# Optimization experiments

Measured on AMD Instinct MI355X. Metric: run time of the kernel, lower is better.

## Reference

```python
import jax, jax.numpy as jnp
import numpy as np

N_NODES = 100000
N_EDGES = 3200000
NUM_GRAPHS = 64
NEG_SLOPE = 0.2  # PyG GATConv default leaky_relu slope


def gat_conv(x, src, dst, W, att_src, att_dst, bias, heads, out_ch, concat):
    """PyG GATConv (default args: add_self_loops=True, negative_slope=0.2).
    src/dst already include self loops."""
    n = x.shape[0]
    h = (x @ W).reshape(n, heads, out_ch)              # [N,H,C]
    a_src = jnp.sum(h * att_src, axis=-1)              # [N,H]
    a_dst = jnp.sum(h * att_dst, axis=-1)              # [N,H]
    e = jax.nn.leaky_relu(a_src[src] + a_dst[dst], NEG_SLOPE)  # [E,H]
    # segment softmax over destination nodes
    m = jax.ops.segment_max(e, dst, num_segments=n)
    ex = jnp.exp(e - m[dst])
    denom = jax.ops.segment_sum(ex, dst, num_segments=n)
    alpha = ex / (denom[dst] + 1e-16)                  # [E,H]
    msg = h[src] * alpha[:, :, None]                   # [E,H,C]
    out = jax.ops.segment_sum(msg, dst, num_segments=n)  # [N,H,C]
    if concat:
        out = out.reshape(n, heads * out_ch)
    else:
        out = out.mean(axis=1)
    return out + bias


def setup_inputs() -> dict:
    key = jax.random.key(0)
    ks = jax.random.split(key, 12)
    x = jax.random.normal(ks[0], (N_NODES, 4), dtype=jnp.float32)
    edge_index = jax.random.randint(ks[1], (2, N_EDGES), 0, N_NODES, dtype=jnp.int64)
    batch = jnp.sort(jax.random.randint(ks[2], (N_NODES,), 0, NUM_GRAPHS, dtype=jnp.int64))
    s = 0.1
    return {
        "x": x,
        "edge_index": edge_index,
        "batch": batch,
        "W1": jax.random.normal(ks[3], (4, 64), dtype=jnp.float32) * s,
        "att_src1": jax.random.normal(ks[4], (2, 32), dtype=jnp.float32) * s,
        "att_dst1": jax.random.normal(ks[5], (2, 32), dtype=jnp.float32) * s,
        "bias1": jnp.zeros((64,), dtype=jnp.float32),
        "W2": jax.random.normal(ks[6], (64, 64), dtype=jnp.float32) * s,
        "att_src2": jax.random.normal(ks[7], (1, 64), dtype=jnp.float32) * s,
        "att_dst2": jax.random.normal(ks[8], (1, 64), dtype=jnp.float32) * s,
        "bias2": jnp.zeros((64,), dtype=jnp.float32),
    }


def reference(x, edge_index, batch, W1, att_src1, att_dst1, bias1, W2, att_src2, att_dst2, bias2):
    n = x.shape[0]
    loops = jnp.arange(n, dtype=edge_index.dtype)
    src = jnp.concatenate([edge_index[0], loops])
    dst = jnp.concatenate([edge_index[1], loops])
    h = gat_conv(x, src, dst, W1, att_src1, att_dst1, bias1, heads=2, out_ch=32, concat=True)
    h = jax.nn.elu(h)
    # dropout is identity in eval mode
    h = gat_conv(h, src, dst, W2, att_src2, att_dst2, bias2, heads=1, out_ch=64, concat=False)
    # global_mean_pool
    sums = jax.ops.segment_sum(h, batch, num_segments=NUM_GRAPHS)
    counts = jax.ops.segment_sum(jnp.ones((n,), h.dtype), batch, num_segments=NUM_GRAPHS)
    return sums / jnp.maximum(counts, 1.0)[:, None]
```

## Files before the change

kernel.cpp:

```cpp
#include <hip/hip_runtime.h>
#include <hip/hip_bf16.h>
#include <hip/hip_fp16.h>
#include <math.h>


__device__ __forceinline__ float leaky(float x) { return x >= 0.f ? x : 0.2f * x; }
__device__ __forceinline__ int iclamp(int v, int lo, int hi) {
  return v < lo ? lo : (v > hi ? hi : v);
}
__device__ __forceinline__ unsigned char f8(float v) {
  return (unsigned char)(__builtin_amdgcn_cvt_pk_fp8_f32(v, v, 0, false) & 0xff);
}
__device__ __forceinline__ float hlo(unsigned w) {
  __half2 h = *(__half2*)&w; return __half2float(h.x);
}
__device__ __forceinline__ float hhi(unsigned w) {
  __half2 h = *(__half2*)&w; return __half2float(h.y);
}

typedef __attribute__((ext_vector_type(8))) _Float16 f16x8;
typedef __attribute__((ext_vector_type(4))) float f32x4;
typedef __attribute__((ext_vector_type(2))) float f32x2;

#define NBUCK 1024
#define BSHIFT 7
#define BCAP 4608
#define CSRSZ (NBUCK * BCAP)
#define MAXR 8
#define SCAP (MAXR * 1024)

__global__ __launch_bounds__(1024, 8) void k_scatt(
    const int* __restrict__ ei, int E, int n, int* __restrict__ bcur,
    unsigned* __restrict__ pairs,
    const float* __restrict__ x, const float* __restrict__ W1,
    const float* __restrict__ att_src1, const float* __restrict__ att_dst1,
    uint4* __restrict__ xs, float* __restrict__ a_dst1, int NBK) {
  __shared__ int h[NBUCK];
  __shared__ int cur[NBUCK];
  __shared__ int gofs[NBUCK];
  __shared__ int wtot[16];
  __shared__ int htot;
  __shared__ unsigned sstage[SCAP];
  __shared__ unsigned short sbkt[SCAP];
  __shared__ float W1s[256];
  __shared__ float as1[64];
  __shared__ float ad1[64];
  int t = threadIdx.x;
  if (blockIdx.x >= NBK) {
    if (t < 256) W1s[t] = W1[t];
    else if (t >= 256 && t < 320) as1[t - 256] = att_src1[t - 256];
    else if (t >= 320 && t < 384) ad1[t - 320] = att_dst1[t - 320];
    __syncthreads();
    int grp = t >> 4, sub = t & 15;
    int node = (blockIdx.x - NBK) * 64 + grp;
    if (node >= n) return;
    float4 xr = ((const float4*)x)[node];
    float vs = 0.f, vd = 0.f;
    #pragma unroll
    for (int i = 0; i < 4; ++i) {
      int c = sub * 4 + i;
      float hv = xr.x * W1s[c] + xr.y * W1s[64 + c] + xr.z * W1s[128 + c] + xr.w * W1s[192 + c];
      vs = fmaf(hv, as1[c], vs);
      vd = fmaf(hv, ad1[c], vd);
    }
    #pragma unroll
    for (int m = 4; m >= 1; m >>= 1) { vs += __shfl_xor(vs, m); vd += __shfl_xor(vd, m); }
    int wl = t & 63;
    float vs1 = __shfl(vs, (wl & 48) + 8);
    float vd1 = __shfl(vd, (wl & 48) + 8);
    if (sub == 0) {
      __half2 x01 = __float22half2_rn(make_float2(xr.x, xr.y));
      __half2 x23 = __float22half2_rn(make_float2(xr.z, xr.w));
      uint4 rec;
      rec.x = *(unsigned*)&x01;
      rec.y = *(unsigned*)&x23;
      rec.z = __float_as_uint(vs);
      rec.w = __float_as_uint(vs1);
      xs[node] = rec;
      ((float2*)a_dst1)[node] = make_float2(vd, vd1);
    }
    return;
  }
  h[t] = 0;
  __syncthreads();
  int chunk = (E + NBK - 1) / NBK;
  int beg = blockIdx.x * chunk;
  int end = beg + chunk; if (end > E) end = E;
  unsigned pR[MAXR];
  unsigned short bR[MAXR];
  int cntr = 0;
  for (int i = beg + t; i < end && cntr < MAXR; i += 1024) {
    int s = iclamp(ei[i], 0, n - 1);
    int d = iclamp(ei[E + i], 0, n - 1);
    int bkt = d >> BSHIFT;
    pR[cntr] = ((unsigned)(d & 127) << 25) | (unsigned)s;
    bR[cntr] = (unsigned short)bkt;
    atomicAdd(&h[bkt], 1);
    ++cntr;
  }
  __syncthreads();
  int v = h[t];
  int lanei = t & 63, wid = t >> 6;
  int sc = v;
  #pragma unroll
  for (int ofs = 1; ofs < 64; ofs <<= 1) {
    int u = __shfl_up(sc, ofs);
    if (lanei >= ofs) sc += u;
  }
  if (lanei == 63) wtot[wid] = sc;
  __syncthreads();
  if (wid == 0 && lanei < 16) {
    int wv = wtot[lanei];
    int s2 = wv;
    #pragma unroll
    for (int ofs = 1; ofs < 16; ofs <<= 1) {
      int u = __shfl_up(s2, ofs);
      if (lanei >= ofs) s2 += u;
    }
    wtot[lanei] = s2 - wv;
  }
  __syncthreads();
  int incl = sc + wtot[wid];
  int loff = incl - v;
  cur[t] = loff;
  gofs[t] = t * BCAP + (v ? atomicAdd(&bcur[t], v) : 0) - loff;
  if (t == 1023) htot = incl;
  __syncthreads();
  for (int k = 0; k < cntr; ++k) {
    int b = bR[k];
    int lpos = atomicAdd(&cur[b], 1);
    sstage[lpos] = pR[k];
    sbkt[lpos] = (unsigned short)b;
  }
  __syncthreads();
  int total = htot;
  for (int i = t; i < total; i += 1024) {
    int b = sbkt[i];
    int pos = gofs[b] + i;
    if (pos >= b * BCAP && pos < (b + 1) * BCAP) pairs[pos] = sstage[i];
  }
}

__global__ __launch_bounds__(256) void k_bgat1(
    const unsigned* __restrict__ pairs, const int* __restrict__ bcur,
    const uint4* __restrict__ xs, const float* __restrict__ W1,
    const float* __restrict__ a_dst1, const float* __restrict__ bias1,
    int* __restrict__ rowbeg, int* __restrict__ rowend, int* __restrict__ csr,
    __half* __restrict__ hB, int n) {
  __shared__ int lcsr[BCAP];
  __shared__ int sh[128];
  __shared__ int cur[128];
  __shared__ int lrb[128];
  __shared__ int lre[128];
  __shared__ int wt[2];
  __shared__ float W1s[256];
  int t = threadIdx.x;
  W1s[t] = W1[t];
  int b = blockIdx.x;
  int node0 = b << BSHIFT;
  if (node0 >= n) return;
  int base = b * BCAP;
  int cnt = iclamp(bcur[b], 0, BCAP);
  if (t < 128) sh[t] = 0;
  __syncthreads();
  for (int i = t; i < cnt; i += 256)
    atomicAdd(&sh[pairs[base + i] >> 25], 1);
  __syncthreads();
  int v = (t < 128) ? sh[t] : 0;
  int lanei = t & 63, wid = t >> 6;
  int sc = v;
  if (wid < 2) {
    #pragma unroll
    for (int ofs = 1; ofs < 64; ofs <<= 1) {
      int u = __shfl_up(sc, ofs);
      if (lanei >= ofs) sc += u;
    }
    if (lanei == 63) wt[wid] = sc;
  }
  __syncthreads();
  if (t < 128) {
    int off = sc + ((wid == 1) ? wt[0] : 0) - v;
    cur[t] = off;
    lrb[t] = off;
    lre[t] = off + v;
    int node = node0 + t;
    if (node < n) {
      rowbeg[node] = base + off;
      rowend[node] = base + off + v;
    }
  }
  __syncthreads();
  for (int i = t; i < cnt; i += 256) {
    unsigned p = pairs[base + i];
    int l = p >> 25;
    int r = atomicAdd(&cur[l], 1);
    if (r >= 0 && r < BCAP) lcsr[r] = (int)(p & 0x1ffffffu);
  }
  __syncthreads();
  for (int i = t; i < cnt; i += 256)
    csr[base + i] = lcsr[i];
  int wave = t >> 6, lane = t & 63;
  int nd = (lane >> 4), sub = lane & 15;
  for (int rnd = 0; rnd < 8; ++rnd) {
    int nodeLocal = rnd * 16 + wave * 4 + nd;
    int node = node0 + nodeLocal;
    bool valid = node < n;
    int nc = valid ? node : 0;
    int ebeg = valid ? lrb[nodeLocal] : 0;
    int eend = valid ? lre[nodeLocal] : 0;
    ebeg = iclamp(ebeg, 0, BCAP);
    eend = iclamp(eend, ebeg, BCAP);
    float2 ad = ((const float2*)a_dst1)[nc];
    uint4 rs = xs[nc];
    float A0 = 0.f, A1 = 0.f, A2 = 0.f, A3 = 0.f, dn0 = 0.f;
    float B0 = 0.f, B1 = 0.f, B2 = 0.f, B3 = 0.f, dn1 = 0.f;
    int e = ebeg + sub;
    for (; e + 16 < eend; e += 32) {
      int sa = iclamp(lcsr[e], 0, n - 1);
      int sb = iclamp(lcsr[e + 16], 0, n - 1);
      uint4 ra = xs[sa];
      uint4 rb = xs[sb];
      float ea0 = __expf(leaky(__uint_as_float(ra.z) + ad.x));
      float ea1 = __expf(leaky(__uint_as_float(ra.w) + ad.y));
      float eb0 = __expf(leaky(__uint_as_float(rb.z) + ad.x));
      float eb1 = __expf(leaky(__uint_as_float(rb.w) + ad.y));
      dn0 += ea0 + eb0; dn1 += ea1 + eb1;
      float xa0 = hlo(ra.x), xa1 = hhi(ra.x), xa2 = hlo(ra.y), xa3 = hhi(ra.y);
      float xb0 = hlo(rb.x), xb1 = hhi(rb.x), xb2 = hlo(rb.y), xb3 = hhi(rb.y);
      A0 = fmaf(ea0, xa0, A0); A1 = fmaf(ea0, xa1, A1);
      A2 = fmaf(ea0, xa2, A2); A3 = fmaf(ea0, xa3, A3);
      B0 = fmaf(ea1, xa0, B0); B1 = fmaf(ea1, xa1, B1);
      B2 = fmaf(ea1, xa2, B2); B3 = fmaf(ea1, xa3, B3);
      A0 = fmaf(eb0, xb0, A0); A1 = fmaf(eb0, xb1, A1);
      A2 = fmaf(eb0, xb2, A2); A3 = fmaf(eb0, xb3, A3);
      B0 = fmaf(eb1, xb0, B0); B1 = fmaf(eb1, xb1, B1);
      B2 = fmaf(eb1, xb2, B2); B3 = fmaf(eb1, xb3, B3);
    }
    if (e < eend) {
      int s = iclamp(lcsr[e], 0, n - 1);
      uint4 rr = xs[s];
      float ex0 = __expf(leaky(__uint_as_float(rr.z) + ad.x));
      float ex1 = __expf(leaky(__uint_as_float(rr.w) + ad.y));
      dn0 += ex0; dn1 += ex1;
      float x0 = hlo(rr.x), x1 = hhi(rr.x), x2 = hlo(rr.y), x3 = hhi(rr.y);
      A0 = fmaf(ex0, x0, A0); A1 = fmaf(ex0, x1, A1);
      A2 = fmaf(ex0, x2, A2); A3 = fmaf(ex0, x3, A3);
      B0 = fmaf(ex1, x0, B0); B1 = fmaf(ex1, x1, B1);
      B2 = fmaf(ex1, x2, B2); B3 = fmaf(ex1, x3, B3);
    }
    bool lo = (sub < 8);
    float C0, C1, C2, C3, dnC, sA, sB;
    sA = __shfl_xor(A0, 8); sB = __shfl_xor(B0, 8); C0 = lo ? A0 + sA : B0 + sB;
    sA = __shfl_xor(A1, 8); sB = __shfl_xor(B1, 8); C1 = lo ? A1 + sA : B1 + sB;
    sA = __shfl_xor(A2, 8); sB = __shfl_xor(B2, 8); C2 = lo ? A2 + sA : B2 + sB;
    sA = __shfl_xor(A3, 8); sB = __shfl_xor(B3, 8); C3 = lo ? A3 + sA : B3 + sB;
    sA = __shfl_xor(dn0, 8); sB = __shfl_xor(dn1, 8); dnC = lo ? dn0 + sA : dn1 + sB;
    #pragma unroll
    for (int m = 4; m >= 1; m >>= 1) {
      C0 += __shfl_xor(C0, m); C1 += __shfl_xor(C1, m);
      C2 += __shfl_xor(C2, m); C3 += __shfl_xor(C3, m);
      dnC += __shfl_xor(dnC, m);
    }
    float exs = __expf(leaky(__uint_as_float(lo ? rs.z : rs.w) + (lo ? ad.x : ad.y)));
    dnC += exs;
    float xs0 = hlo(rs.x), xs1 = hhi(rs.x), xs2 = hlo(rs.y), xs3 = hhi(rs.y);
    C0 = fmaf(exs, xs0, C0); C1 = fmaf(exs, xs1, C1);
    C2 = fmaf(exs, xs2, C2); C3 = fmaf(exs, xs3, C3);
    float inv = 1.0f / (dnC + 1e-16f);
    if (valid) {
      int f0 = sub * 4;
      float vv[4];
      #pragma unroll
      for (int i = 0; i < 4; ++i) {
        int f = f0 + i;
        float accv = C0 * W1s[f] + C1 * W1s[64 + f] + C2 * W1s[128 + f] + C3 * W1s[192 + f];
        float vx = accv * inv + bias1[f];
        vv[i] = vx > 0.f ? vx : expm1f(vx);
      }
      __half2 h01 = __float22half2_rn(make_float2(vv[0], vv[1]));
      __half2 h23 = __float22half2_rn(make_float2(vv[2], vv[3]));
      uint2 pk;
      pk.x = *(unsigned*)&h01;
      pk.y = *(unsigned*)&h23;
      *(uint2*)(hB + (size_t)node * 64 + f0) = pk;
    }
  }
}

__global__ __launch_bounds__(256) void k_lin2(
    const __half* __restrict__ hB, const float* __restrict__ W2,
    const float* __restrict__ att_src2, const float* __restrict__ att_dst2,
    float* __restrict__ a_src2, float* __restrict__ a_dst2,
    unsigned char* __restrict__ hC, int n) {
  __shared__ __attribute__((aligned(16))) _Float16 Whi[64 * 72];
  __shared__ __attribute__((aligned(16))) _Float16 Wlo[64 * 72];
  int t = threadIdx.x;
  for (int i = t; i < 4096; i += 256) {
    int k = i >> 6, col = i & 63;
    float w = W2[i];
    _Float16 hi = (_Float16)w;
    _Float16 lo = (_Float16)(w - (float)hi);
    Whi[col * 72 + k] = hi;
    Wlo[col * 72 + k] = lo;
  }
  __syncthreads();
  int wave = t >> 6, lane = t & 63;
  int quad = lane >> 4, c = lane & 15;
  float as2[4], ad2[4];
  #pragma unroll
  for (int tt = 0; tt < 4; ++tt) {
    as2[tt] = att_src2[tt * 16 + c];
    ad2[tt] = att_dst2[tt * 16 + c];
  }
  for (int it = 0; it < 4; ++it) {
    int m0 = blockIdx.x * 256 + wave * 64 + it * 16;
    if (m0 >= n) break;
    int mrow = m0 + c; if (mrow > n - 1) mrow = n - 1;
    const _Float16* hrow = (const _Float16*)(hB + (size_t)mrow * 64);
    f16x8 a0 = *(const f16x8*)(hrow + quad * 8);
    f16x8 a1 = *(const f16x8*)(hrow + 32 + quad * 8);
    f32x4 zero = {0.f, 0.f, 0.f, 0.f};
    f32x4 acc[4] = {zero, zero, zero, zero};
    #pragma unroll
    for (int tt = 0; tt < 4; ++tt) {
      int nn = tt * 16 + c;
      const _Float16* wh = &Whi[nn * 72];
      const _Float16* wl = &Wlo[nn * 72];
      f16x8 bh0 = *(const f16x8*)(wh + quad * 8);
      f16x8 bh1 = *(const f16x8*)(wh + 32 + quad * 8);
      f16x8 bl0 = *(const f16x8*)(wl + quad * 8);
      f16x8 bl1 = *(const f16x8*)(wl + 32 + quad * 8);
      acc[tt] = __builtin_amdgcn_mfma_f32_16x16x32_f16(a0, bh0, acc[tt], 0, 0, 0);
      acc[tt] = __builtin_amdgcn_mfma_f32_16x16x32_f16(a1, bh1, acc[tt], 0, 0, 0);
      acc[tt] = __builtin_amdgcn_mfma_f32_16x16x32_f16(a0, bl0, acc[tt], 0, 0, 0);
      acc[tt] = __builtin_amdgcn_mfma_f32_16x16x32_f16(a1, bl1, acc[tt], 0, 0, 0);
    }
    #pragma unroll
    for (int r = 0; r < 4; ++r) {
      float s = 0.f, d = 0.f;
      #pragma unroll
      for (int tt = 0; tt < 4; ++tt) {
        s = fmaf(acc[tt][r], as2[tt], s);
        d = fmaf(acc[tt][r], ad2[tt], d);
      }
      #pragma unroll
      for (int msk = 8; msk >= 1; msk >>= 1) {
        s += __shfl_xor(s, msk);
        d += __shfl_xor(d, msk);
      }
      int m = m0 + quad * 4 + r;
      if (m < n) {
        if (c == 0) { a_src2[m] = s; a_dst2[m] = d; }
        unsigned char* orow = hC + (size_t)m * 64;
        #pragma unroll
        for (int tt = 0; tt < 4; ++tt)
          orow[tt * 16 + c] = f8(acc[tt][r]);
      }
    }
  }
}

#define ACC8(HW, EE) do { \
    f32x2 _a = __builtin_amdgcn_cvt_pk_f32_fp8((HW).x, false); \
    f32x2 _b = __builtin_amdgcn_cvt_pk_f32_fp8((HW).x, true); \
    ac0 = fmaf((EE), _a.x, ac0); ac1 = fmaf((EE), _a.y, ac1); \
    ac2 = fmaf((EE), _b.x, ac2); ac3 = fmaf((EE), _b.y, ac3); \
    _a = __builtin_amdgcn_cvt_pk_f32_fp8((HW).y, false); \
    _b = __builtin_amdgcn_cvt_pk_f32_fp8((HW).y, true); \
    ac4 = fmaf((EE), _a.x, ac4); ac5 = fmaf((EE), _a.y, ac5); \
    ac6 = fmaf((EE), _b.x, ac6); ac7 = fmaf((EE), _b.y, ac7); \
  } while (0)

__global__ __launch_bounds__(256) void k_gat2(
    const unsigned char* __restrict__ hC, const float* __restrict__ a_src2,
    const float* __restrict__ a_dst2, const int* __restrict__ rowbeg,
    const int* __restrict__ rowend, const int* __restrict__ csr,
    const float* __restrict__ bias2,
    __half* __restrict__ h2, int n) {
  __shared__ unsigned long long stage[4 * 64];
  int t = threadIdx.x;
  int w = t >> 6, lane = t & 63;
  int node = blockIdx.x * 4 + w;
  if (node >= n) return;
  int beg = iclamp(rowbeg[node], 0, CSRSZ);
  int end = iclamp(rowend[node], beg, CSRSZ);
  float ad = a_dst2[node];
  int g = lane >> 3;
  int p = lane & 7;
  const uint2* hrows = (const uint2*)hC;
  unsigned long long* st = &stage[w * 64];
  float ac0 = 0.f, ac1 = 0.f, ac2 = 0.f, ac3 = 0.f;
  float ac4 = 0.f, ac5 = 0.f, ac6 = 0.f, ac7 = 0.f;
  float dn = 0.f;
  for (int tb = beg; tb < end; tb += 64) {
    int tc = end - tb; if (tc > 64) tc = 64;
    int s = 0; float ex = 0.f;
    if (lane < tc) {
      s = iclamp(csr[tb + lane], 0, n - 1);
      ex = __expf(leaky(a_src2[s] + ad));
    }
    dn += ex;
    st[lane] = ((unsigned long long)(unsigned)s << 32) | (unsigned)__float_as_uint(ex);
    int steps = (tc + 7) >> 3;
    int j = 0;
    for (; j + 4 <= steps; j += 4) {
      unsigned long long pk0 = st[(j + 0) * 8 + g];
      unsigned long long pk1 = st[(j + 1) * 8 + g];
      unsigned long long pk2 = st[(j + 2) * 8 + g];
      unsigned long long pk3 = st[(j + 3) * 8 + g];
      int s0 = (int)(pk0 >> 32), s1 = (int)(pk1 >> 32);
      int s2 = (int)(pk2 >> 32), s3 = (int)(pk3 >> 32);
      float e0 = __uint_as_float((unsigned)pk0);
      float e1 = __uint_as_float((unsigned)pk1);
      float e2 = __uint_as_float((unsigned)pk2);
      float e3 = __uint_as_float((unsigned)pk3);
      uint2 hw0 = hrows[(size_t)s0 * 8 + p];
      uint2 hw1 = hrows[(size_t)s1 * 8 + p];
      uint2 hw2 = hrows[(size_t)s2 * 8 + p];
      uint2 hw3 = hrows[(size_t)s3 * 8 + p];
      ACC8(hw0, e0);
      ACC8(hw1, e1);
      ACC8(hw2, e2);
      ACC8(hw3, e3);
    }
    for (; j < steps; ++j) {
      unsigned long long pk0 = st[j * 8 + g];
      int s0 = (int)(pk0 >> 32);
      float e0 = __uint_as_float((unsigned)pk0);
      uint2 hw0 = hrows[(size_t)s0 * 8 + p];
      ACC8(hw0, e0);
    }
  }
  #pragma unroll
  for (int m = 8; m <= 32; m <<= 1) {
    ac0 += __shfl_xor(ac0, m); ac1 += __shfl_xor(ac1, m);
    ac2 += __shfl_xor(ac2, m); ac3 += __shfl_xor(ac3, m);
    ac4 += __shfl_xor(ac4, m); ac5 += __shfl_xor(ac5, m);
    ac6 += __shfl_xor(ac6, m); ac7 += __shfl_xor(ac7, m);
  }
  #pragma unroll
  for (int m = 32; m >= 1; m >>= 1) dn += __shfl_xor(dn, m);
  float exs = __expf(leaky(a_src2[node] + ad));
  dn += exs;
  uint2 hs = hrows[(size_t)node * 8 + p];
  ACC8(hs, exs);
  if (g == 0) {
    float inv = 1.0f / (dn + 1e-16f);
    const float* b2 = bias2 + p * 8;
    __half2 o0 = __float22half2_rn(make_float2(ac0 * inv + b2[0], ac1 * inv + b2[1]));
    __half2 o1 = __float22half2_rn(make_float2(ac2 * inv + b2[2], ac3 * inv + b2[3]));
    __half2 o2 = __float22half2_rn(make_float2(ac4 * inv + b2[4], ac5 * inv + b2[5]));
    __half2 o3 = __float22half2_rn(make_float2(ac6 * inv + b2[6], ac7 * inv + b2[7]));
    uint4 pk;
    pk.x = *(unsigned*)&o0; pk.y = *(unsigned*)&o1;
    pk.z = *(unsigned*)&o2; pk.w = *(unsigned*)&o3;
    ((uint4*)(h2 + (size_t)node * 64))[p] = pk;
  }
}

__global__ __launch_bounds__(256) void k_pool(
    const __half* __restrict__ h2, const int* __restrict__ batch,
    float* __restrict__ pool, float* __restrict__ cnt, int n, int G) {
  const int PW = 64;
  int wave = blockIdx.x * 4 + (threadIdx.x >> 6);
  int lane = threadIdx.x & 63;
  int start = wave * PW;
  if (start < n) {
    int end = start + PW; if (end > n) end = n;
    int bcur = iclamp(batch[start], 0, G - 1);
    float acc = 0.f, count = 0.f;
    for (int i = start; i < end; ++i) {
      int b = iclamp(batch[i], 0, G - 1);
      if (b != bcur) {
        atomicAdd(&pool[bcur * 64 + lane], acc);
        if (lane == 0) atomicAdd(&cnt[bcur], count);
        bcur = b; acc = 0.f; count = 0.f;
      }
      acc += __half2float(h2[(size_t)i * 64 + lane]);
      count += 1.f;
    }
    atomicAdd(&pool[bcur * 64 + lane], acc);
    if (lane == 0) atomicAdd(&cnt[bcur], count);
  }
}

__global__ void k_final(const float* __restrict__ pool, const float* __restrict__ cnt,
                        float* __restrict__ out, int G) {
  int i = blockIdx.x * blockDim.x + threadIdx.x;
  if (i >= G * 64) return;
  out[i] = pool[i] / fmaxf(cnt[i >> 6], 1.0f);
}

extern "C" void kernel_launch(void* const* d_in, const int* in_sizes, int n_in,
                              void* d_out, int out_size, void* d_ws, size_t ws_size,
                              hipStream_t stream) {
  const float* x        = (const float*)d_in[0];
  const int*   ei       = (const int*)d_in[1];
  const int*   batch    = (const int*)d_in[2];
  const float* W1       = (const float*)d_in[3];
  const float* att_src1 = (const float*)d_in[4];
  const float* att_dst1 = (const float*)d_in[5];
  const float* bias1    = (const float*)d_in[6];
  const float* W2       = (const float*)d_in[7];
  const float* att_src2 = (const float*)d_in[8];
  const float* att_dst2 = (const float*)d_in[9];
  const float* bias2    = (const float*)d_in[10];

  const int n = in_sizes[0] / 4;
  const int E = in_sizes[1] / 2;
  const int G = out_size / 64;

  char* p = (char*)d_ws;
  auto alloc = [&](size_t bytes) -> void* {
    void* r = (void*)p;
    p += (bytes + 255) & ~(size_t)255;
    return r;
  };
  unsigned* pairs = (unsigned*)alloc((size_t)CSRSZ * 4);
  int* csr = (int*)pairs;
  size_t hsz = (size_t)n * 64 * 2;
  char* R = (char*)alloc(hsz + (size_t)n * 64);
  __half* hB = (__half*)R;
  __half* h2 = (__half*)R;
  unsigned char* hC = (unsigned char*)(R + hsz);
  uint4* xs     = (uint4*)alloc((size_t)n * 16);
  int*   rowbeg = (int*)alloc((size_t)n * 4);
  int*   rowend = (int*)alloc((size_t)n * 4);
  size_t poolelems = (size_t)G * 64 + G;
  char*  Z = (char*)alloc(poolelems * 4 + (size_t)NBUCK * 4);
  float* pool = (float*)Z;
  float* cnt  = pool + (size_t)G * 64;
  int*   bcur = (int*)(Z + poolelems * 4);
  float* a_dst1 = (float*)alloc((size_t)n * 2 * 4);
  float* a_src2 = (float*)alloc((size_t)n * 4);
  float* a_dst2 = (float*)alloc((size_t)n * 4);

  hipMemsetAsync(Z, 0, poolelems * 4 + (size_t)NBUCK * 4, stream);

  int NBK = (E + MAXR * 1024 - 1) / (MAXR * 1024);
  if (NBK < 512) NBK = 512;
  int natt = (n + 63) / 64;

  k_scatt<<<NBK + natt, 1024, 0, stream>>>(ei, E, n, bcur, pairs,
                                           x, W1, att_src1, att_dst1, xs, a_dst1, NBK);
  k_bgat1<<<NBUCK, 256, 0, stream>>>(pairs, bcur, xs, W1, a_dst1, bias1,
                                     rowbeg, rowend, csr, hB, n);
  k_lin2<<<(n + 255) / 256, 256, 0, stream>>>(hB, W2, att_src2, att_dst2, a_src2, a_dst2, hC, n);
  k_gat2<<<(n + 3) / 4, 256, 0, stream>>>(hC, a_src2, a_dst2, rowbeg, rowend, csr, bias2, h2, n);
  k_pool<<<(n + 255) / 256, 256, 0, stream>>>(h2, batch, pool, cnt, n, G);
  k_final<<<(G * 64 + 255) / 256, 256, 0, stream>>>(pool, cnt, (float*)d_out, G);
}
```

Baseline: 244.9 us.

## Vectorize edge loads in scatter, stage pairs in LDS, split gat2 launch

The scatter kernel now has each thread read two edges at once with int2 loads, and the per-block chunk is rounded to an even size. The bucket CSR kernel copies its pairs into an LDS array on the first pass so the second pass reads shared memory instead of global memory again. The gat2 kernel is split into two launches over the two halves of the nodes. The costs are extra LDS per block, which can lower occupancy, an extra launch, and possible misaligned int2 loads if E is odd.

Result: no change. 248.1 us (+1.3%).

```diff
diff --git a/kernel.cpp b/kernel.cpp
--- a/kernel.cpp
+++ b/kernel.cpp
@@ -84,19 +84,43 @@
   h[t] = 0;
   __syncthreads();
   int chunk = (E + NBK - 1) / NBK;
+  chunk = (chunk + 1) & ~1;
   int beg = blockIdx.x * chunk;
   int end = beg + chunk; if (end > E) end = E;
   unsigned pR[MAXR];
   unsigned short bR[MAXR];
   int cntr = 0;
-  for (int i = beg + t; i < end && cntr < MAXR; i += 1024) {
-    int s = iclamp(ei[i], 0, n - 1);
-    int d = iclamp(ei[E + i], 0, n - 1);
-    int bkt = d >> BSHIFT;
-    pR[cntr] = ((unsigned)(d & 127) << 25) | (unsigned)s;
-    bR[cntr] = (unsigned short)bkt;
-    atomicAdd(&h[bkt], 1);
-    ++cntr;
+  for (int i = beg + 2 * t; i < end && cntr < MAXR; i += 2048) {
+    if (i + 1 < end) {
+      int2 sv = *(const int2*)(ei + i);
+      int2 dv = *(const int2*)(ei + E + i);
+      {
+        int s = iclamp(sv.x, 0, n - 1);
+        int d = iclamp(dv.x, 0, n - 1);
+        int bkt = d >> BSHIFT;
+        pR[cntr] = ((unsigned)(d & 127) << 25) | (unsigned)s;
+        bR[cntr] = (unsigned short)bkt;
+        atomicAdd(&h[bkt], 1);
+        ++cntr;
+      }
+      if (cntr < MAXR) {
+        int s = iclamp(sv.y, 0, n - 1);
+        int d = iclamp(dv.y, 0, n - 1);
+        int bkt = d >> BSHIFT;
+        pR[cntr] = ((unsigned)(d & 127) << 25) | (unsigned)s;
+        bR[cntr] = (unsigned short)bkt;
+        atomicAdd(&h[bkt], 1);
+        ++cntr;
+      }
+    } else {
+      int s = iclamp(ei[i], 0, n - 1);
+      int d = iclamp(ei[E + i], 0, n - 1);
+      int bkt = d >> BSHIFT;
+      pR[cntr] = ((unsigned)(d & 127) << 25) | (unsigned)s;
+      bR[cntr] = (unsigned short)bkt;
+      atomicAdd(&h[bkt], 1);
+      ++cntr;
+    }
   }
   __syncthreads();
   int v = h[t];
@@ -148,6 +172,7 @@
     int* __restrict__ rowbeg, int* __restrict__ rowend, int* __restrict__ csr,
     __half* __restrict__ hB, int n) {
   __shared__ int lcsr[BCAP];
+  __shared__ int praw[BCAP];
   __shared__ int sh[128];
   __shared__ int cur[128];
   __shared__ int lrb[128];
@@ -163,8 +188,11 @@
   int cnt = iclamp(bcur[b], 0, BCAP);
   if (t < 128) sh[t] = 0;
   __syncthreads();
-  for (int i = t; i < cnt; i += 256)
-    atomicAdd(&sh[pairs[base + i] >> 25], 1);
+  for (int i = t; i < cnt; i += 256) {
+    int pv = (int)pairs[base + i];
+    praw[i] = pv;
+    atomicAdd(&sh[((unsigned)pv) >> 25], 1);
+  }
   __syncthreads();
   int v = (t < 128) ? sh[t] : 0;
   int lanei = t & 63, wid = t >> 6;
@@ -191,7 +219,7 @@
   }
   __syncthreads();
   for (int i = t; i < cnt; i += 256) {
-    unsigned p = pairs[base + i];
+    unsigned p = (unsigned)praw[i];
     int l = p >> 25;
     int r = atomicAdd(&cur[l], 1);
     if (r >= 0 && r < BCAP) lcsr[r] = (int)(p & 0x1ffffffu);
@@ -376,11 +404,11 @@
     const float* __restrict__ a_dst2, const int* __restrict__ rowbeg,
     const int* __restrict__ rowend, const int* __restrict__ csr,
     const float* __restrict__ bias2,
-    __half* __restrict__ h2, int n) {
+    __half* __restrict__ h2, int n, int node0) {
   __shared__ unsigned long long stage[4 * 64];
   int t = threadIdx.x;
   int w = t >> 6, lane = t & 63;
-  int node = blockIdx.x * 4 + w;
+  int node = node0 + blockIdx.x * 4 + w;
   if (node >= n) return;
   int beg = iclamp(rowbeg[node], 0, CSRSZ);
   int end = iclamp(rowend[node], beg, CSRSZ);
@@ -546,7 +574,11 @@
   k_bgat1<<<NBUCK, 256, 0, stream>>>(pairs, bcur, xs, W1, a_dst1, bias1,
                                      rowbeg, rowend, csr, hB, n);
   k_lin2<<<(n + 255) / 256, 256, 0, stream>>>(hB, W2, att_src2, att_dst2, a_src2, a_dst2, hC, n);
-  k_gat2<<<(n + 3) / 4, 256, 0, stream>>>(hC, a_src2, a_dst2, rowbeg, rowend, csr, bias2, h2, n);
+  int nh = ((n / 2) + 3) & ~3;
+  if (nh > n) nh = n;
+  k_gat2<<<(nh + 3) / 4, 256, 0, stream>>>(hC, a_src2, a_dst2, rowbeg, rowend, csr, bias2, h2, n, 0);
+  if (n > nh)
+    k_gat2<<<(n - nh + 3) / 4, 256, 0, stream>>>(hC, a_src2, a_dst2, rowbeg, rowend, csr, bias2, h2, n, nh);
   k_pool<<<(n + 255) / 256, 256, 0, stream>>>(h2, batch, pool, cnt, n, G);
   k_final<<<(G * 64 + 255) / 256, 256, 0, stream>>>(pool, cnt, (float*)d_out, G);
 }
```
